# Kernel tuning notes

Measured on AMD Instinct MI355X. Metric: run time of the kernel, lower is better.

The kernel has to match this reference:

```python
import jax, jax.numpy as jnp
import numpy as np

DIM, DEPTH, HEADS, DIM_HEAD, MLP_DIM = 512, 6, 8, 64, 2048
INNER = HEADS * DIM_HEAD
EPS = 1e-5


def _layernorm(x, s, b):
    mu = jnp.mean(x, axis=-1, keepdims=True)
    var = jnp.mean(jnp.square(x - mu), axis=-1, keepdims=True)
    return (x - mu) * jax.lax.rsqrt(var + EPS) * s + b


def setup_inputs() -> dict:
    key = jax.random.key(0)
    ks = jax.random.split(key, 12)
    d = {
        "x": jax.random.normal(ks[0], (8, 1024, DIM), dtype=jnp.float32),
        "ln1_s": jnp.ones((DEPTH, DIM), jnp.float32),
        "ln1_b": jnp.zeros((DEPTH, DIM), jnp.float32),
        "w_qkv": jax.random.normal(ks[1], (DEPTH, DIM, 3 * INNER), dtype=jnp.float32) * (DIM ** -0.5),
        "w_out": jax.random.normal(ks[2], (DEPTH, INNER, DIM), dtype=jnp.float32) * (INNER ** -0.5),
        "b_out": jnp.zeros((DEPTH, DIM), jnp.float32),
        "ln2_s": jnp.ones((DEPTH, DIM), jnp.float32),
        "ln2_b": jnp.zeros((DEPTH, DIM), jnp.float32),
        "w1": jax.random.normal(ks[3], (DEPTH, DIM, MLP_DIM), dtype=jnp.float32) * (DIM ** -0.5),
        "b1": jnp.zeros((DEPTH, MLP_DIM), jnp.float32),
        "w2": jax.random.normal(ks[4], (DEPTH, MLP_DIM, DIM), dtype=jnp.float32) * (MLP_DIM ** -0.5),
        "b2": jnp.zeros((DEPTH, DIM), jnp.float32),
    }
    return d


def reference(x, ln1_s, ln1_b, w_qkv, w_out, b_out, ln2_s, ln2_b, w1, b1, w2, b2):
    b, n, _ = x.shape
    scale = DIM_HEAD ** -0.5
    for i in range(DEPTH):
        # --- PreNorm Attention with residual ---
        h = _layernorm(x, ln1_s[i], ln1_b[i])
        qkv = h @ w_qkv[i]                                  # [b, n, 3*inner]
        q, k, v = jnp.split(qkv, 3, axis=-1)
        q = q.reshape(b, n, HEADS, DIM_HEAD)
        k = k.reshape(b, n, HEADS, DIM_HEAD)
        v = v.reshape(b, n, HEADS, DIM_HEAD)
        dots = jnp.einsum('bihd,bjhd->bhij', q, k) * scale  # [b, h, n, n]
        attn = jax.nn.softmax(dots, axis=-1)
        out = jnp.einsum('bhij,bjhd->bihd', attn, v).reshape(b, n, INNER)
        x = out @ w_out[i] + b_out[i] + x
        # --- PreNorm FeedForward with residual ---
        h = _layernorm(x, ln2_s[i], ln2_b[i])
        h = jax.nn.gelu(h @ w1[i] + b1[i], approximate=False)
        x = h @ w2[i] + b2[i] + x
    return x
```

## Files before the change

### kernel.cpp

```cpp
#include <hip/hip_runtime.h>
#include <cstdint>
#include <cstddef>

#define M_TOK 8192
#define DIMM  512
#define HEADS 8
#define DH    64
#define MLPD  2048
#define DEPTH 6

typedef unsigned short u16;
typedef unsigned int   u32;
typedef __attribute__((ext_vector_type(8))) short short8;
typedef __attribute__((ext_vector_type(4))) float f32x4;

__device__ __forceinline__ float bf2f(u16 u){ return __uint_as_float(((u32)u) << 16); }
__device__ __forceinline__ u16 f2bf(float f){
    u32 x = __float_as_uint(f);
    u32 r = x + 0x7fffu + ((x >> 16) & 1u);
    return (u16)(r >> 16);
}
__device__ __forceinline__ u32 cvt_pk_bf16(float a, float b){
    u32 r;
    asm("v_cvt_pk_bf16_f32 %0, %1, %2" : "=v"(r) : "v"(a), "v"(b));
    return r;
}
__device__ __forceinline__ void async16(const u16* g, u16* l){
    __builtin_amdgcn_global_load_lds(
        (const __attribute__((address_space(1))) void*)(uintptr_t)(const void*)g,
        (__attribute__((address_space(3))) void*)(u32)(uintptr_t)(void*)l,
        16, 0, 0);
}
__device__ __forceinline__ void xcd_swizzle(int& bx, int& by){
    int nbx = gridDim.x, nby = gridDim.y;
    if ((nby & 7) == 0){
        int i = by * nbx + bx;
        int xcd = i & 7, j = i >> 3, ypg = nby >> 3;
        int yq = j / nbx;
        by = xcd * ypg + yq;
        bx = j - yq * nbx;
    }
}

__global__ void k_transpose_cvt(const float* __restrict__ in, u16* __restrict__ out, int R, int C){
    __shared__ u16 tile[32][33];
    size_t zoff = (size_t)blockIdx.z * R * C;
    in += zoff; out += zoff;
    int c0 = blockIdx.x * 32, r0 = blockIdx.y * 32;
    int tx = threadIdx.x, ty = threadIdx.y;
    #pragma unroll
    for (int i = 0; i < 32; i += 8)
        tile[ty + i][tx] = f2bf(in[(size_t)(r0 + ty + i) * C + c0 + tx]);
    __syncthreads();
    #pragma unroll
    for (int i = 0; i < 32; i += 8)
        out[(size_t)(c0 + ty + i) * R + r0 + tx] = tile[tx][ty + i];
}

__global__ __launch_bounds__(256) void k_layernorm(const float* __restrict__ x,
                                                   const float* __restrict__ s,
                                                   const float* __restrict__ b,
                                                   u16* __restrict__ out){
    int row = blockIdx.x * 4 + (threadIdx.x >> 6);
    int lane = threadIdx.x & 63;
    const float* xp = x + (size_t)row * DIMM + lane * 8;
    float v[8];
    #pragma unroll
    for (int c = 0; c < 8; c++) v[c] = xp[c];
    float sum = 0.f, sq = 0.f;
    #pragma unroll
    for (int c = 0; c < 8; c++){ sum += v[c]; sq += v[c] * v[c]; }
    #pragma unroll
    for (int m = 32; m >= 1; m >>= 1){
        sum += __shfl_xor(sum, m);
        sq  += __shfl_xor(sq,  m);
    }
    float mu  = sum * (1.f / DIMM);
    float var = sq * (1.f / DIMM) - mu * mu;
    float rs  = rsqrtf(var + 1e-5f);
    u16* op = out + (size_t)row * DIMM + lane * 8;
    #pragma unroll
    for (int c = 0; c < 8; c++){
        int col = lane * 8 + c;
        op[c] = f2bf((v[c] - mu) * rs * s[col] + b[col]);
    }
}

__device__ __forceinline__ float erf_as(float x){
    float ax = fabsf(x);
    float t  = __builtin_amdgcn_rcpf(fmaf(0.3275911f, ax, 1.f));
    float y  = fmaf(fmaf(fmaf(fmaf(1.061405429f, t, -1.453152027f), t,
                              1.421413741f), t, -0.284496736f), t, 0.254829592f) * t;
    float e  = exp2f(-ax * ax * 1.4426950408889634f);
    float r  = 1.f - y * e;
    return copysignf(r, x);
}
__device__ __forceinline__ float gelu_exact(float v){
    return 0.5f * v * (1.f + erf_as(v * 0.70710678118654752f));
}

#define LDT64 72

template<int MODE>
__global__ __launch_bounds__(256) void k_gemm128b(const u16* __restrict__ A,
                                                  const u16* __restrict__ Bt,
                                                  const float* __restrict__ bias,
                                                  u16* __restrict__ Cout,
                                                  int M, int N, int K){
    __shared__ u16 As[2][128 * 64];
    __shared__ u16 Bs[2][128 * 64];
    int bx = blockIdx.x, by = blockIdx.y;
    xcd_swizzle(bx, by);
    int m0 = by * 128, n0 = bx * 128;
    int t = threadIdx.x;
    int w = t >> 6, lane = t & 63;
    int mi = lane & 15, quad = lane >> 4;
    int wr = w >> 1, wc = w & 1;

    int grow = lane >> 3, gcol = (lane & 7) * 8;
    const u16* agl = A  + (size_t)(m0 + w * 32 + grow) * K + gcol;
    const u16* bgl = Bt + (size_t)(n0 + w * 32 + grow) * K + gcol;

    f32x4 acc[4][4];
    #pragma unroll
    for (int mt = 0; mt < 4; mt++)
        #pragma unroll
        for (int nt = 0; nt < 4; nt++) acc[mt][nt] = (f32x4){0.f, 0.f, 0.f, 0.f};

    int nt_k = K >> 6;
    {
        u16* asl = &As[0][(w * 32) * 64];
        u16* bsl = &Bs[0][(w * 32) * 64];
        #pragma unroll
        for (int i = 0; i < 4; i++){
            async16(agl + (size_t)(i * 8) * K, asl + i * 8 * 64);
            async16(bgl + (size_t)(i * 8) * K, bsl + i * 8 * 64);
        }
    }
    __syncthreads();

    for (int td = 0; td < nt_k; td++){
        int cur = td & 1;
        if (td + 1 < nt_k){
            int k0 = (td + 1) << 6;
            u16* asl = &As[cur ^ 1][(w * 32) * 64];
            u16* bsl = &Bs[cur ^ 1][(w * 32) * 64];
            #pragma unroll
            for (int i = 0; i < 4; i++){
                async16(agl + (size_t)(i * 8) * K + k0, asl + i * 8 * 64);
                async16(bgl + (size_t)(i * 8) * K + k0, bsl + i * 8 * 64);
            }
        }
        const u16* Ab = &As[cur][0];
        const u16* Bb = &Bs[cur][0];
        #pragma unroll
        for (int kk = 0; kk < 64; kk += 32){
            short8 af[4], bf[4];
            #pragma unroll
            for (int mt = 0; mt < 4; mt++)
                af[mt] = *(const short8*)&Ab[(wr * 64 + mt * 16 + mi) * 64 + kk + quad * 8];
            #pragma unroll
            for (int nt = 0; nt < 4; nt++)
                bf[nt] = *(const short8*)&Bb[(wc * 64 + nt * 16 + mi) * 64 + kk + quad * 8];
            #pragma unroll
            for (int mt = 0; mt < 4; mt++)
                #pragma unroll
                for (int nt = 0; nt < 4; nt++)
                    acc[mt][nt] = __builtin_amdgcn_mfma_f32_16x16x32_bf16(af[mt], bf[nt], acc[mt][nt], 0, 0, 0);
        }
        __syncthreads();
    }

    float bv[4];
    if (MODE == 1){
        #pragma unroll
        for (int nt = 0; nt < 4; nt++) bv[nt] = bias[n0 + wc * 64 + nt * 16 + mi];
    }
    u16* cs = ((u16*)As) + w * 16 * LDT64;
    int erow = lane >> 2, ecol = (lane & 3) * 16;
    #pragma unroll
    for (int mt = 0; mt < 4; mt++){
        #pragma unroll
        for (int nt = 0; nt < 4; nt++)
            #pragma unroll
            for (int r = 0; r < 4; r++){
                float v = acc[mt][nt][r];
                if (MODE == 1) v = gelu_exact(v + bv[nt]);
                cs[(quad * 4 + r) * LDT64 + nt * 16 + mi] = f2bf(v);
            }
        uint4 c0 = *(const uint4*)&cs[erow * LDT64 + ecol];
        uint4 c1 = *(const uint4*)&cs[erow * LDT64 + ecol + 8];
        u16* cp = Cout + (size_t)(m0 + wr * 64 + mt * 16 + erow) * N + n0 + wc * 64 + ecol;
        *(uint4*)cp       = c0;
        *(uint4*)(cp + 8) = c1;
    }
}

__global__ __launch_bounds__(256) void k_gemm128_res(const u16* __restrict__ A,
                                                     const u16* __restrict__ Bt,
                                                     const float* __restrict__ bias,
                                                     float* __restrict__ xres,
                                                     int M, int N, int K){
    __shared__ u16 As[2][128 * 64];
    __shared__ u16 Bs[2][128 * 64];
    int bx = blockIdx.x, by = blockIdx.y;
    xcd_swizzle(bx, by);
    int m0 = by * 128, n0 = bx * 128;
    int t = threadIdx.x;
    int w = t >> 6, lane = t & 63;
    int mi = lane & 15, quad = lane >> 4;
    int wr = w >> 1, wc = w & 1;

    int grow = lane >> 3, gcol = (lane & 7) * 8;
    const u16* agl = A  + (size_t)(m0 + w * 32 + grow) * K + gcol;
    const u16* bgl = Bt + (size_t)(n0 + w * 32 + grow) * K + gcol;

    f32x4 acc[4][4];
    #pragma unroll
    for (int mt = 0; mt < 4; mt++)
        #pragma unroll
        for (int nt = 0; nt < 4; nt++) acc[mt][nt] = (f32x4){0.f, 0.f, 0.f, 0.f};

    int nt_k = K >> 6;
    {
        u16* asl = &As[0][(w * 32) * 64];
        u16* bsl = &Bs[0][(w * 32) * 64];
        #pragma unroll
        for (int i = 0; i < 4; i++){
            async16(agl + (size_t)(i * 8) * K, asl + i * 8 * 64);
            async16(bgl + (size_t)(i * 8) * K, bsl + i * 8 * 64);
        }
    }
    __syncthreads();

    for (int td = 0; td < nt_k; td++){
        int cur = td & 1;
        if (td + 1 < nt_k){
            int k0 = (td + 1) << 6;
            u16* asl = &As[cur ^ 1][(w * 32) * 64];
            u16* bsl = &Bs[cur ^ 1][(w * 32) * 64];
            #pragma unroll
            for (int i = 0; i < 4; i++){
                async16(agl + (size_t)(i * 8) * K + k0, asl + i * 8 * 64);
                async16(bgl + (size_t)(i * 8) * K + k0, bsl + i * 8 * 64);
            }
        }
        const u16* Ab = &As[cur][0];
        const u16* Bb = &Bs[cur][0];
        #pragma unroll
        for (int kk = 0; kk < 64; kk += 32){
            short8 af[4], bf[4];
            #pragma unroll
            for (int mt = 0; mt < 4; mt++)
                af[mt] = *(const short8*)&Ab[(wr * 64 + mt * 16 + mi) * 64 + kk + quad * 8];
            #pragma unroll
            for (int nt = 0; nt < 4; nt++)
                bf[nt] = *(const short8*)&Bb[(wc * 64 + nt * 16 + mi) * 64 + kk + quad * 8];
            #pragma unroll
            for (int mt = 0; mt < 4; mt++)
                #pragma unroll
                for (int nt = 0; nt < 4; nt++)
                    acc[mt][nt] = __builtin_amdgcn_mfma_f32_16x16x32_bf16(af[mt], bf[nt], acc[mt][nt], 0, 0, 0);
        }
        __syncthreads();
    }

    float bv[4];
    #pragma unroll
    for (int nt = 0; nt < 4; nt++) bv[nt] = bias[n0 + wc * 64 + nt * 16 + mi];
    float* cs = ((float*)As) + w * 16 * LDT64;
    int erow = lane >> 2, ecol = (lane & 3) * 16;
    #pragma unroll
    for (int mt = 0; mt < 4; mt++){
        #pragma unroll
        for (int nt = 0; nt < 4; nt++)
            #pragma unroll
            for (int r = 0; r < 4; r++)
                cs[(quad * 4 + r) * LDT64 + nt * 16 + mi] = acc[mt][nt][r] + bv[nt];
        float* xp = xres + (size_t)(m0 + wr * 64 + mt * 16 + erow) * N + n0 + wc * 64 + ecol;
        #pragma unroll
        for (int j = 0; j < 4; j++){
            float4 cv = *(const float4*)&cs[erow * LDT64 + ecol + j * 4];
            float4 xv = *(const float4*)(xp + j * 4);
            xv.x += cv.x; xv.y += cv.y; xv.z += cv.z; xv.w += cv.w;
            *(float4*)(xp + j * 4) = xv;
        }
    }
}

#define LDK 72
#define C1_LOG2E 0.18033688011112042f
#define C2_LOG2E 11.541560327111707f
#define OSPLIT (M_TOK * 512)
#define LSPLIT (M_TOK * 8)

__global__ __launch_bounds__(256) void k_flash_split(const u16* __restrict__ qkv,
                                                     float* __restrict__ Opart,
                                                     float* __restrict__ lpart){
    __shared__ u16 Ks[64 * LDK];
    __shared__ u16 Vt[80 * LDK];
    __shared__ u16 Ps[4][32 * LDK];
    int wg = (blockIdx.x & 7) * 128 + (blockIdx.x >> 3);
    int qt = wg & 7, h = (wg >> 3) & 7, sp = (wg >> 6) & 1, b = wg >> 7;
    int t = threadIdx.x;
    int w = t >> 6, lane = t & 63;
    int mi = lane & 15, quad = lane >> 4;

    for (int i = t; i < 16 * 64; i += 256){
        int d = i >> 6, kk = i & 63;
        Vt[(64 + d) * LDK + kk] = 0x3F80;
    }

    const u16* base = qkv + ((size_t)b * 1024) * 1536;
    int hoff = h * 64;

    short8 qf[2][2];
    #pragma unroll
    for (int qh = 0; qh < 2; qh++){
        int qrow = qt * 128 + w * 32 + qh * 16 + mi;
        const u16* qp = base + (size_t)qrow * 1536 + hoff + quad * 8;
        qf[qh][0] = *(const short8*)(qp);
        qf[qh][1] = *(const short8*)(qp + 32);
    }

    f32x4 o[2][4];
    f32x4 lacc[2];
    #pragma unroll
    for (int qh = 0; qh < 2; qh++){
        #pragma unroll
        for (int nb = 0; nb < 4; nb++) o[qh][nb] = (f32x4){0.f, 0.f, 0.f, 0.f};
        lacc[qh] = (f32x4){0.f, 0.f, 0.f, 0.f};
    }

    int kkey = t >> 2, kseg = t & 3;
    const u16* kgp = base + (size_t)kkey * 1536 + 512 + hoff + kseg * 16;
    int vkey = lane, vdg = w;
    const u16* vgp = base + (size_t)vkey * 1536 + 1024 + hoff + vdg * 16;

    int kt0 = sp * 8;
    size_t koff0 = (size_t)kt0 * 64 * 1536;
    uint4 kv0 = *(const uint4*)(kgp + koff0);
    uint4 kv1 = *(const uint4*)(kgp + koff0 + 8);
    uint4 vv0 = *(const uint4*)(vgp + koff0);
    uint4 vv1 = *(const uint4*)(vgp + koff0 + 8);

    for (int kt = kt0; kt < kt0 + 8; kt++){
        __syncthreads();
        *(uint4*)&Ks[kkey * LDK + kseg * 16]     = kv0;
        *(uint4*)&Ks[kkey * LDK + kseg * 16 + 8] = kv1;
        u16 vtmp[16];
        *(uint4*)&vtmp[0] = vv0;
        *(uint4*)&vtmp[8] = vv1;
        #pragma unroll
        for (int i = 0; i < 16; i++)
            Vt[(vdg * 16 + i) * LDK + vkey] = vtmp[i];
        __syncthreads();

        if (kt < kt0 + 7){
            size_t koff = (size_t)(kt + 1) * 64 * 1536;
            kv0 = *(const uint4*)(kgp + koff);
            kv1 = *(const uint4*)(kgp + koff + 8);
            vv0 = *(const uint4*)(vgp + koff);
            vv1 = *(const uint4*)(vgp + koff + 8);
        }

        short8 kb[4][2];
        #pragma unroll
        for (int nb = 0; nb < 4; nb++){
            kb[nb][0] = *(const short8*)&Ks[(nb * 16 + mi) * LDK + quad * 8];
            kb[nb][1] = *(const short8*)&Ks[(nb * 16 + mi) * LDK + quad * 8 + 32];
        }
        #pragma unroll
        for (int qh = 0; qh < 2; qh++){
            #pragma unroll
            for (int nb = 0; nb < 4; nb++){
                f32x4 z = (f32x4){0.f, 0.f, 0.f, 0.f};
                z = __builtin_amdgcn_mfma_f32_16x16x32_bf16(qf[qh][0], kb[nb][0], z, 0, 0, 0);
                z = __builtin_amdgcn_mfma_f32_16x16x32_bf16(qf[qh][1], kb[nb][1], z, 0, 0, 0);
                float e0 = exp2f(fmaf(z[0], C1_LOG2E, -C2_LOG2E));
                float e1 = exp2f(fmaf(z[1], C1_LOG2E, -C2_LOG2E));
                float e2 = exp2f(fmaf(z[2], C1_LOG2E, -C2_LOG2E));
                float e3 = exp2f(fmaf(z[3], C1_LOG2E, -C2_LOG2E));
                u32 p01 = cvt_pk_bf16(e0, e1);
                u32 p23 = cvt_pk_bf16(e2, e3);
                u16* pp = &Ps[w][(qh * 16 + quad * 4) * LDK + nb * 16 + mi];
                pp[0]       = (u16)p01;
                pp[LDK]     = (u16)(p01 >> 16);
                pp[2 * LDK] = (u16)p23;
                pp[3 * LDK] = (u16)(p23 >> 16);
            }
        }
        short8 vb[4][2], lb[2];
        #pragma unroll
        for (int nb = 0; nb < 4; nb++){
            vb[nb][0] = *(const short8*)&Vt[(nb * 16 + mi) * LDK + quad * 8];
            vb[nb][1] = *(const short8*)&Vt[(nb * 16 + mi) * LDK + quad * 8 + 32];
        }
        lb[0] = *(const short8*)&Vt[(64 + mi) * LDK + quad * 8];
        lb[1] = *(const short8*)&Vt[(64 + mi) * LDK + quad * 8 + 32];
        #pragma unroll
        for (int qh = 0; qh < 2; qh++){
            const short8 a0 = *(const short8*)&Ps[w][(qh * 16 + mi) * LDK + quad * 8];
            const short8 a1 = *(const short8*)&Ps[w][(qh * 16 + mi) * LDK + quad * 8 + 32];
            #pragma unroll
            for (int nb = 0; nb < 4; nb++){
                o[qh][nb] = __builtin_amdgcn_mfma_f32_16x16x32_bf16(a0, vb[nb][0], o[qh][nb], 0, 0, 0);
                o[qh][nb] = __builtin_amdgcn_mfma_f32_16x16x32_bf16(a1, vb[nb][1], o[qh][nb], 0, 0, 0);
            }
            lacc[qh] = __builtin_amdgcn_mfma_f32_16x16x32_bf16(a0, lb[0], lacc[qh], 0, 0, 0);
            lacc[qh] = __builtin_amdgcn_mfma_f32_16x16x32_bf16(a1, lb[1], lacc[qh], 0, 0, 0);
        }
    }
    float* Ob = Opart + (size_t)sp * OSPLIT;
    float* lb2 = lpart + (size_t)sp * LSPLIT;
    #pragma unroll
    for (int qh = 0; qh < 2; qh++){
        int grow0 = b * 1024 + qt * 128 + w * 32 + qh * 16;
        float* op = Ob + (size_t)grow0 * 512 + hoff;
        #pragma unroll
        for (int nb = 0; nb < 4; nb++)
            #pragma unroll
            for (int r = 0; r < 4; r++)
                op[(size_t)(quad * 4 + r) * 512 + nb * 16 + mi] = o[qh][nb][r];
        if (mi == 0){
            #pragma unroll
            for (int r = 0; r < 4; r++)
                lb2[(size_t)(grow0 + quad * 4 + r) * 8 + h] = lacc[qh][r];
        }
    }
}

__global__ __launch_bounds__(256) void k_combine(const float* __restrict__ Opart,
                                                 const float* __restrict__ lpart,
                                                 u16* __restrict__ out){
    int tid = blockIdx.x * 256 + threadIdx.x;
    size_t basei = (size_t)tid * 8;
    int row = (int)(basei >> 9), col = (int)(basei & 511), h = col >> 6;
    float l = lpart[(size_t)row * 8 + h] + lpart[(size_t)LSPLIT + (size_t)row * 8 + h];
    float inv = 1.f / l;
    float4 a0 = *(const float4*)(Opart + basei);
    float4 a1 = *(const float4*)(Opart + basei + 4);
    float4 b0 = *(const float4*)(Opart + (size_t)OSPLIT + basei);
    float4 b1 = *(const float4*)(Opart + (size_t)OSPLIT + basei + 4);
    uint4 r;
    r.x = cvt_pk_bf16((a0.x + b0.x) * inv, (a0.y + b0.y) * inv);
    r.y = cvt_pk_bf16((a0.z + b0.z) * inv, (a0.w + b0.w) * inv);
    r.z = cvt_pk_bf16((a1.x + b1.x) * inv, (a1.y + b1.y) * inv);
    r.w = cvt_pk_bf16((a1.z + b1.z) * inv, (a1.w + b1.w) * inv);
    *(uint4*)(out + basei) = r;
}

__global__ __launch_bounds__(256) void k_flash(const u16* __restrict__ qkv, u16* __restrict__ out){
    __shared__ u16 Ks[64 * LDK];
    __shared__ u16 Vt[80 * LDK];
    __shared__ u16 Ps[4][32 * LDK];
    int wg = (blockIdx.x & 7) * 64 + (blockIdx.x >> 3);
    int qt = wg & 7, h = (wg >> 3) & 7, b = wg >> 6;
    int t = threadIdx.x;
    int w = t >> 6, lane = t & 63;
    int mi = lane & 15, quad = lane >> 4;

    for (int i = t; i < 16 * 64; i += 256){
        int d = i >> 6, kk = i & 63;
        Vt[(64 + d) * LDK + kk] = 0x3F80;
    }
    const u16* base = qkv + ((size_t)b * 1024) * 1536;
    int hoff = h * 64;

    short8 qf[2][2];
    #pragma unroll
    for (int qh = 0; qh < 2; qh++){
        int qrow = qt * 128 + w * 32 + qh * 16 + mi;
        const u16* qp = base + (size_t)qrow * 1536 + hoff + quad * 8;
        qf[qh][0] = *(const short8*)(qp);
        qf[qh][1] = *(const short8*)(qp + 32);
    }
    f32x4 o[2][4];
    f32x4 lacc[2];
    #pragma unroll
    for (int qh = 0; qh < 2; qh++){
        #pragma unroll
        for (int nb = 0; nb < 4; nb++) o[qh][nb] = (f32x4){0.f, 0.f, 0.f, 0.f};
        lacc[qh] = (f32x4){0.f, 0.f, 0.f, 0.f};
    }
    int kkey = t >> 2, kseg = t & 3;
    const u16* kgp = base + (size_t)kkey * 1536 + 512 + hoff + kseg * 16;
    int vkey = lane, vdg = w;
    const u16* vgp = base + (size_t)vkey * 1536 + 1024 + hoff + vdg * 16;

    uint4 kv0 = *(const uint4*)(kgp);
    uint4 kv1 = *(const uint4*)(kgp + 8);
    uint4 vv0 = *(const uint4*)(vgp);
    uint4 vv1 = *(const uint4*)(vgp + 8);

    for (int kt = 0; kt < 16; kt++){
        __syncthreads();
        *(uint4*)&Ks[kkey * LDK + kseg * 16]     = kv0;
        *(uint4*)&Ks[kkey * LDK + kseg * 16 + 8] = kv1;
        u16 vtmp[16];
        *(uint4*)&vtmp[0] = vv0;
        *(uint4*)&vtmp[8] = vv1;
        #pragma unroll
        for (int i = 0; i < 16; i++)
            Vt[(vdg * 16 + i) * LDK + vkey] = vtmp[i];
        __syncthreads();
        if (kt < 15){
            size_t koff = (size_t)(kt + 1) * 64 * 1536;
            kv0 = *(const uint4*)(kgp + koff);
            kv1 = *(const uint4*)(kgp + koff + 8);
            vv0 = *(const uint4*)(vgp + koff);
            vv1 = *(const uint4*)(vgp + koff + 8);
        }
        short8 kb[4][2];
        #pragma unroll
        for (int nb = 0; nb < 4; nb++){
            kb[nb][0] = *(const short8*)&Ks[(nb * 16 + mi) * LDK + quad * 8];
            kb[nb][1] = *(const short8*)&Ks[(nb * 16 + mi) * LDK + quad * 8 + 32];
        }
        #pragma unroll
        for (int qh = 0; qh < 2; qh++){
            #pragma unroll
            for (int nb = 0; nb < 4; nb++){
                f32x4 z = (f32x4){0.f, 0.f, 0.f, 0.f};
                z = __builtin_amdgcn_mfma_f32_16x16x32_bf16(qf[qh][0], kb[nb][0], z, 0, 0, 0);
                z = __builtin_amdgcn_mfma_f32_16x16x32_bf16(qf[qh][1], kb[nb][1], z, 0, 0, 0);
                float e0 = exp2f(fmaf(z[0], C1_LOG2E, -C2_LOG2E));
                float e1 = exp2f(fmaf(z[1], C1_LOG2E, -C2_LOG2E));
                float e2 = exp2f(fmaf(z[2], C1_LOG2E, -C2_LOG2E));
                float e3 = exp2f(fmaf(z[3], C1_LOG2E, -C2_LOG2E));
                u32 p01 = cvt_pk_bf16(e0, e1);
                u32 p23 = cvt_pk_bf16(e2, e3);
                u16* pp = &Ps[w][(qh * 16 + quad * 4) * LDK + nb * 16 + mi];
                pp[0]       = (u16)p01;
                pp[LDK]     = (u16)(p01 >> 16);
                pp[2 * LDK] = (u16)p23;
                pp[3 * LDK] = (u16)(p23 >> 16);
            }
        }
        short8 vb[4][2], lb[2];
        #pragma unroll
        for (int nb = 0; nb < 4; nb++){
            vb[nb][0] = *(const short8*)&Vt[(nb * 16 + mi) * LDK + quad * 8];
            vb[nb][1] = *(const short8*)&Vt[(nb * 16 + mi) * LDK + quad * 8 + 32];
        }
        lb[0] = *(const short8*)&Vt[(64 + mi) * LDK + quad * 8];
        lb[1] = *(const short8*)&Vt[(64 + mi) * LDK + quad * 8 + 32];
        #pragma unroll
        for (int qh = 0; qh < 2; qh++){
            const short8 a0 = *(const short8*)&Ps[w][(qh * 16 + mi) * LDK + quad * 8];
            const short8 a1 = *(const short8*)&Ps[w][(qh * 16 + mi) * LDK + quad * 8 + 32];
            #pragma unroll
            for (int nb = 0; nb < 4; nb++){
                o[qh][nb] = __builtin_amdgcn_mfma_f32_16x16x32_bf16(a0, vb[nb][0], o[qh][nb], 0, 0, 0);
                o[qh][nb] = __builtin_amdgcn_mfma_f32_16x16x32_bf16(a1, vb[nb][1], o[qh][nb], 0, 0, 0);
            }
            lacc[qh] = __builtin_amdgcn_mfma_f32_16x16x32_bf16(a0, lb[0], lacc[qh], 0, 0, 0);
            lacc[qh] = __builtin_amdgcn_mfma_f32_16x16x32_bf16(a1, lb[1], lacc[qh], 0, 0, 0);
        }
    }
    #pragma unroll
    for (int qh = 0; qh < 2; qh++){
        float invl[4];
        #pragma unroll
        for (int r = 0; r < 4; r++) invl[r] = 1.f / lacc[qh][r];
        u16* op = out + ((size_t)b * 1024 + qt * 128 + w * 32 + qh * 16) * 512 + hoff;
        #pragma unroll
        for (int nb = 0; nb < 4; nb++){
            u32 c01 = cvt_pk_bf16(o[qh][nb][0] * invl[0], o[qh][nb][1] * invl[1]);
            u32 c23 = cvt_pk_bf16(o[qh][nb][2] * invl[2], o[qh][nb][3] * invl[3]);
            u16* cp = op + (size_t)(quad * 4) * 512 + nb * 16 + mi;
            cp[0]       = (u16)c01;
            cp[512]     = (u16)(c01 >> 16);
            cp[2 * 512] = (u16)c23;
            cp[3 * 512] = (u16)(c23 >> 16);
        }
    }
}

extern "C" void kernel_launch(void* const* d_in, const int* in_sizes, int n_in,
                              void* d_out, int out_size, void* d_ws, size_t ws_size,
                              hipStream_t stream){
    const float* x_in  = (const float*)d_in[0];
    const float* ln1_s = (const float*)d_in[1];
    const float* ln1_b = (const float*)d_in[2];
    const float* w_qkv = (const float*)d_in[3];
    const float* w_out = (const float*)d_in[4];
    const float* b_out = (const float*)d_in[5];
    const float* ln2_s = (const float*)d_in[6];
    const float* ln2_b = (const float*)d_in[7];
    const float* w1    = (const float*)d_in[8];
    const float* b1    = (const float*)d_in[9];
    const float* w2    = (const float*)d_in[10];
    const float* b2    = (const float*)d_in[11];
    float* out = (float*)d_out;

    char* ws = (char*)d_ws;
    float* x_f32 = (float*)ws;   ws += (size_t)M_TOK * DIMM * 4;
    u16* bufA    = (u16*)ws;     ws += (size_t)M_TOK * DIMM * 2;
    u16* bufB    = (u16*)ws;     ws += (size_t)M_TOK * MLPD * 2;

    size_t per_layer_w = (size_t)(1536 + 512 + 2048 + 2048) * 512;
    size_t split_bytes = (size_t)2 * OSPLIT * 4 + (size_t)2 * LSPLIT * 4;
    size_t base_used = (size_t)(ws - (char*)d_ws);

    bool split_ok = ws_size >= base_used + split_bytes + per_layer_w * 2;
    float* Opart = (float*)ws;
    float* lpart = (float*)(ws + (size_t)2 * OSPLIT * 4);
    u16* wbase = split_ok ? (u16*)(ws + split_bytes) : (u16*)ws;
    size_t wb_off = (size_t)((char*)wbase - (char*)d_ws);
    bool big = ws_size >= wb_off + per_layer_w * 2 * DEPTH;

    u16* ln_out   = bufA;
    u16* attn_out = bufA;
    u16* qkv      = bufB;
    u16* mlp_h    = bufB;

    size_t x_bytes = (size_t)M_TOK * DIMM * sizeof(float);
    hipMemcpyAsync(x_f32, x_in, x_bytes, hipMemcpyDeviceToDevice, stream);

    const size_t off_qkv = 0;
    const size_t off_out = (size_t)1536 * 512;
    const size_t off_w1  = off_out + (size_t)512 * 512;
    const size_t off_w2  = off_w1 + (size_t)2048 * 512;

    if (big){
        k_transpose_cvt<<<dim3(48, 16, 6), dim3(32, 8), 0, stream>>>(w_qkv, wbase + off_qkv * DEPTH, 512, 1536);
        k_transpose_cvt<<<dim3(16, 16, 6), dim3(32, 8), 0, stream>>>(w_out, wbase + off_out * DEPTH, 512, 512);
        k_transpose_cvt<<<dim3(64, 16, 6), dim3(32, 8), 0, stream>>>(w1,    wbase + off_w1  * DEPTH, 512, 2048);
        k_transpose_cvt<<<dim3(16, 64, 6), dim3(32, 8), 0, stream>>>(w2,    wbase + off_w2  * DEPTH, 2048, 512);
    }

    for (int i = 0; i < DEPTH; i++){
        u16 *wqkvT, *woutT, *w1T, *w2T;
        if (big){
            wqkvT = wbase + off_qkv * DEPTH + (size_t)i * 1536 * 512;
            woutT = wbase + off_out * DEPTH + (size_t)i * 512 * 512;
            w1T   = wbase + off_w1  * DEPTH + (size_t)i * 2048 * 512;
            w2T   = wbase + off_w2  * DEPTH + (size_t)i * 512 * 2048;
        } else {
            wqkvT = wbase + off_qkv; woutT = wbase + off_out;
            w1T   = wbase + off_w1;  w2T   = wbase + off_w2;
            k_transpose_cvt<<<dim3(48, 16), dim3(32, 8), 0, stream>>>(w_qkv + (size_t)i * 512 * 1536, wqkvT, 512, 1536);
            k_transpose_cvt<<<dim3(16, 16), dim3(32, 8), 0, stream>>>(w_out + (size_t)i * 512 * 512,  woutT, 512, 512);
            k_transpose_cvt<<<dim3(64, 16), dim3(32, 8), 0, stream>>>(w1    + (size_t)i * 512 * 2048, w1T,   512, 2048);
            k_transpose_cvt<<<dim3(16, 64), dim3(32, 8), 0, stream>>>(w2    + (size_t)i * 2048 * 512, w2T,   2048, 512);
        }

        k_layernorm<<<dim3(M_TOK / 4), dim3(256), 0, stream>>>(x_f32, ln1_s + i * 512, ln1_b + i * 512, ln_out);
        k_gemm128b<0><<<dim3(12, 64), dim3(256), 0, stream>>>(ln_out, wqkvT, nullptr, qkv,
                                                              M_TOK, 1536, 512);
        if (split_ok){
            k_flash_split<<<dim3(1024), dim3(256), 0, stream>>>(qkv, Opart, lpart);
            k_combine<<<dim3(2048), dim3(256), 0, stream>>>(Opart, lpart, attn_out);
        } else {
            k_flash<<<dim3(512), dim3(256), 0, stream>>>(qkv, attn_out);
        }
        k_gemm128_res<<<dim3(4, 64), dim3(256), 0, stream>>>(attn_out, woutT, b_out + i * 512, x_f32,
                                                             M_TOK, 512, 512);
        k_layernorm<<<dim3(M_TOK / 4), dim3(256), 0, stream>>>(x_f32, ln2_s + i * 512, ln2_b + i * 512, ln_out);
        k_gemm128b<1><<<dim3(16, 64), dim3(256), 0, stream>>>(ln_out, w1T, b1 + i * 2048, mlp_h,
                                                              M_TOK, 2048, 512);
        k_gemm128_res<<<dim3(4, 64), dim3(256), 0, stream>>>(mlp_h, w2T, b2 + i * 512, x_f32,
                                                             M_TOK, 512, 2048);
    }
    hipMemcpyAsync(out, x_f32, x_bytes, hipMemcpyDeviceToDevice, stream);
}
```

Baseline: 1.153 ms.

## Swizzle GEMM LDS tiles with XOR and use vmcnt-based waits instead of syncthreads

Both 128x128 GEMM kernels now write global-to-LDS async loads into an XOR-swizzled column layout (chunk ^ row&7) and read fragments with the matching swizzle. This is meant to remove LDS bank conflicts on the short8 fragment reads. The full __syncthreads after each prefetch is replaced by an s_waitcnt vmcnt(8) plus a raw s_barrier, so the next tile's loads stay in flight while the current tile is consumed. The risk is correctness if the vmcnt count does not match the number of outstanding async loads, or if the swizzle mapping disagrees between the writers and readers.

New measurement: 1.093 ms. 1.05x faster.

```diff
diff --git a/kernel.cpp b/kernel.cpp
--- a/kernel.cpp
+++ b/kernel.cpp
@@ -116,8 +116,10 @@
     int w = t >> 6, lane = t & 63;
     int mi = lane & 15, quad = lane >> 4;
     int wr = w >> 1, wc = w & 1;
-
-    int grow = lane >> 3, gcol = (lane & 7) * 8;
+    int sw = mi & 7;
+
+    int grow = lane >> 3;
+    int gcol = (((lane & 7) ^ grow) & 7) * 8;
     const u16* agl = A  + (size_t)(m0 + w * 32 + grow) * K + gcol;
     const u16* bgl = Bt + (size_t)(n0 + w * 32 + grow) * K + gcol;
 
@@ -137,7 +139,6 @@
             async16(bgl + (size_t)(i * 8) * K, bsl + i * 8 * 64);
         }
     }
-    __syncthreads();
 
     for (int td = 0; td < nt_k; td++){
         int cur = td & 1;
@@ -150,25 +151,32 @@
                 async16(agl + (size_t)(i * 8) * K + k0, asl + i * 8 * 64);
                 async16(bgl + (size_t)(i * 8) * K + k0, bsl + i * 8 * 64);
             }
-        }
+            asm volatile("s_waitcnt vmcnt(8)" ::: "memory");
+        } else {
+            asm volatile("s_waitcnt vmcnt(0)" ::: "memory");
+        }
+        __builtin_amdgcn_s_barrier();
+        __builtin_amdgcn_sched_barrier(0);
         const u16* Ab = &As[cur][0];
         const u16* Bb = &Bs[cur][0];
         #pragma unroll
         for (int kk = 0; kk < 64; kk += 32){
+            const int kc = kk >> 3;
             short8 af[4], bf[4];
             #pragma unroll
             for (int mt = 0; mt < 4; mt++)
-                af[mt] = *(const short8*)&Ab[(wr * 64 + mt * 16 + mi) * 64 + kk + quad * 8];
+                af[mt] = *(const short8*)&Ab[(wr * 64 + mt * 16 + mi) * 64 + (((quad + kc) ^ sw) * 8)];
             #pragma unroll
             for (int nt = 0; nt < 4; nt++)
-                bf[nt] = *(const short8*)&Bb[(wc * 64 + nt * 16 + mi) * 64 + kk + quad * 8];
+                bf[nt] = *(const short8*)&Bb[(wc * 64 + nt * 16 + mi) * 64 + (((quad + kc) ^ sw) * 8)];
             #pragma unroll
             for (int mt = 0; mt < 4; mt++)
                 #pragma unroll
                 for (int nt = 0; nt < 4; nt++)
                     acc[mt][nt] = __builtin_amdgcn_mfma_f32_16x16x32_bf16(af[mt], bf[nt], acc[mt][nt], 0, 0, 0);
         }
-        __syncthreads();
+        __builtin_amdgcn_sched_barrier(0);
+        __builtin_amdgcn_s_barrier();
     }
 
     float bv[4];
@@ -210,8 +218,10 @@
     int w = t >> 6, lane = t & 63;
     int mi = lane & 15, quad = lane >> 4;
     int wr = w >> 1, wc = w & 1;
-
-    int grow = lane >> 3, gcol = (lane & 7) * 8;
+    int sw = mi & 7;
+
+    int grow = lane >> 3;
+    int gcol = (((lane & 7) ^ grow) & 7) * 8;
     const u16* agl = A  + (size_t)(m0 + w * 32 + grow) * K + gcol;
     const u16* bgl = Bt + (size_t)(n0 + w * 32 + grow) * K + gcol;
 
@@ -231,7 +241,6 @@
             async16(bgl + (size_t)(i * 8) * K, bsl + i * 8 * 64);
         }
     }
-    __syncthreads();
 
     for (int td = 0; td < nt_k; td++){
         int cur = td & 1;
@@ -244,25 +253,32 @@
                 async16(agl + (size_t)(i * 8) * K + k0, asl + i * 8 * 64);
                 async16(bgl + (size_t)(i * 8) * K + k0, bsl + i * 8 * 64);
             }
-        }
+            asm volatile("s_waitcnt vmcnt(8)" ::: "memory");
+        } else {
+            asm volatile("s_waitcnt vmcnt(0)" ::: "memory");
+        }
+        __builtin_amdgcn_s_barrier();
+        __builtin_amdgcn_sched_barrier(0);
         const u16* Ab = &As[cur][0];
         const u16* Bb = &Bs[cur][0];
         #pragma unroll
         for (int kk = 0; kk < 64; kk += 32){
+            const int kc = kk >> 3;
             short8 af[4], bf[4];
             #pragma unroll
             for (int mt = 0; mt < 4; mt++)
-                af[mt] = *(const short8*)&Ab[(wr * 64 + mt * 16 + mi) * 64 + kk + quad * 8];
+                af[mt] = *(const short8*)&Ab[(wr * 64 + mt * 16 + mi) * 64 + (((quad + kc) ^ sw) * 8)];
             #pragma unroll
             for (int nt = 0; nt < 4; nt++)
-                bf[nt] = *(const short8*)&Bb[(wc * 64 + nt * 16 + mi) * 64 + kk + quad * 8];
+                bf[nt] = *(const short8*)&Bb[(wc * 64 + nt * 16 + mi) * 64 + (((quad + kc) ^ sw) * 8)];
             #pragma unroll
             for (int mt = 0; mt < 4; mt++)
                 #pragma unroll
                 for (int nt = 0; nt < 4; nt++)
                     acc[mt][nt] = __builtin_amdgcn_mfma_f32_16x16x32_bf16(af[mt], bf[nt], acc[mt][nt], 0, 0, 0);
         }
-        __syncthreads();
+        __builtin_amdgcn_sched_barrier(0);
+        __builtin_amdgcn_s_barrier();
     }
 
     float bv[4];
```
